# Kernel tuning notes

Hardware: AMD Instinct MI355X
Metric: run time of the kernel (lower is better)

Reference implementation:

```python
import jax, jax.numpy as jnp
import numpy as np

D = 512
H = 8
DV = D // H  # 64
NEG_INF = -1e30


def setup_inputs() -> dict:
    key = jax.random.key(0)
    ks = jax.random.split(key, 10)
    B, S = 4, 2048
    x = jax.random.normal(ks[0], (B, D, S), dtype=jnp.float32)
    mask = jnp.ones((B, S), dtype=jnp.float32)
    s = 1.0 / np.sqrt(D)
    sv = 1.0 / np.sqrt(D)
    # per-head Linear(d -> dv) weights stacked: [H, dv, d] (torch Linear layout W @ x)
    Wq = jax.random.uniform(ks[1], (H, DV, D), jnp.float32, -s, s)
    bq = jax.random.uniform(ks[2], (H, DV), jnp.float32, -s, s)
    Wk = jax.random.uniform(ks[3], (H, DV, D), jnp.float32, -s, s)
    bk = jax.random.uniform(ks[4], (H, DV), jnp.float32, -s, s)
    Wv = jax.random.uniform(ks[5], (H, DV, D), jnp.float32, -s, s)
    bv = jax.random.uniform(ks[6], (H, DV), jnp.float32, -s, s)
    W0 = jax.random.uniform(ks[7], (D, D), jnp.float32, -sv, sv)
    b0 = jax.random.uniform(ks[8], (D,), jnp.float32, -sv, sv)
    return {"x": x, "mask": mask, "Wq": Wq, "bq": bq, "Wk": Wk, "bk": bk,
            "Wv": Wv, "bv": bv, "W0": W0, "b0": b0}


def reference(x, mask, Wq, bq, Wk, bk, Wv, bv, W0, b0):
    # x: [B, d, S] -> xt: [B, S, d]
    xt = jnp.transpose(x, (0, 2, 1))
    # fused per-head projections: [B, H, S, dv]
    q = jnp.einsum('bsd,hed->bhse', xt, Wq) + bq[None, :, None, :]
    k = jnp.einsum('bsd,hed->bhse', xt, Wk) + bk[None, :, None, :]
    v = jnp.einsum('bsd,hed->bhse', xt, Wv) + bv[None, :, None, :]
    dv = q.shape[-1]
    scores = jnp.einsum('bhse,bhte->bhst', q, k) * (1.0 / np.sqrt(dv))
    # mask_logits (QANet style): keep where mask==1, else -1e30; mask over key dim
    h_mask = mask[:, None, None, :]  # [B,1,1,S]
    scores = scores * h_mask + (1.0 - h_mask) * NEG_INF
    p = jax.nn.softmax(scores, axis=-1)
    # zero out fully-masked query rows via v_mask on query dim
    p = p * mask[:, None, :, None]
    out = jnp.einsum('bhst,bhte->bhse', p, v)  # [B,H,S,dv]
    # concat heads along feature dim -> [B, S, d]
    B, _, S, _ = out.shape
    heads = jnp.transpose(out, (0, 2, 1, 3)).reshape(B, S, -1)
    y = heads @ W0.T + b0  # output projection
    return jnp.transpose(y, (0, 2, 1))  # [B, d, S]
```

## Files before the change

kernel.cpp:

```cpp
#include <hip/hip_runtime.h>

#define B_  4
#define D_  512
#define H_  8
#define DV_ 64
#define S_  2048
#define LOG2E 1.442695041f

typedef __bf16 bf16;
typedef bf16  bf16x8 __attribute__((ext_vector_type(8)));
typedef bf16  bf16x4 __attribute__((ext_vector_type(4)));
typedef float f32x4  __attribute__((ext_vector_type(4)));

#define MFMA(a, b, c) __builtin_amdgcn_mfma_f32_16x16x32_bf16((a), (b), (c), 0, 0, 0)

#define GLOAD_LDS(g, l)                                                     \
    __builtin_amdgcn_global_load_lds(                                       \
        (const __attribute__((address_space(1))) void*)(g),                 \
        (__attribute__((address_space(3))) void*)(l), 16, 0, 0)

#define WAIT_VMCNT(n)                                                       \
    __builtin_amdgcn_s_waitcnt(((n) & 15) | (((n) >> 4) << 14) | (7 << 4) | (15 << 8))

__global__ __launch_bounds__(256) void prep(
    const float* __restrict__ x, const float* __restrict__ Wq,
    const float* __restrict__ Wk, const float* __restrict__ Wv,
    const float* __restrict__ W0, bf16* __restrict__ xb, bf16* __restrict__ Wb) {
    const int bid = blockIdx.x;
    if (bid < 4096) {
        __shared__ float tile[32][33];
        const int sblk = bid % 64;
        const int dblk = (bid / 64) % 16;
        const int b    = bid / 1024;
        const int d0 = dblk * 32, s0 = sblk * 32;
        const int tx = threadIdx.x & 31;
        const int ty = threadIdx.x >> 5;
        const float* xp = x + (size_t)b * D_ * S_;
#pragma unroll
        for (int i = 0; i < 32; i += 8)
            tile[ty + i][tx] = xp[(size_t)(d0 + ty + i) * S_ + s0 + tx];
        __syncthreads();
        bf16* xbp = xb + ((size_t)b * S_ + s0) * D_ + d0;
        const int srow = threadIdx.x >> 3;
        const int d4   = (threadIdx.x & 7) * 4;
        bf16x4 hv;
#pragma unroll
        for (int j = 0; j < 4; ++j) hv[j] = (bf16)tile[d4 + j][srow];
        *(bf16x4*)&xbp[(size_t)srow * D_ + d4] = hv;
    } else {
        const int f0 = ((bid - 4096) * 256 + threadIdx.x) * 16;
        const int src = f0 >> 18;
        const int off = f0 & 262143;
        const float* W = (src == 0) ? Wq : (src == 1) ? Wk : (src == 2) ? Wv : W0;
        float4 v0 = *(const float4*)&W[off];
        float4 v1 = *(const float4*)&W[off + 4];
        float4 v2 = *(const float4*)&W[off + 8];
        float4 v3 = *(const float4*)&W[off + 12];
        bf16x8 h0 = {(bf16)v0.x, (bf16)v0.y, (bf16)v0.z, (bf16)v0.w,
                     (bf16)v1.x, (bf16)v1.y, (bf16)v1.z, (bf16)v1.w};
        bf16x8 h1 = {(bf16)v2.x, (bf16)v2.y, (bf16)v2.z, (bf16)v2.w,
                     (bf16)v3.x, (bf16)v3.y, (bf16)v3.z, (bf16)v3.w};
        *(bf16x8*)&Wb[f0]     = h0;
        *(bf16x8*)&Wb[f0 + 8] = h1;
    }
}

__global__ __launch_bounds__(256) void gemm_qkv(
    const bf16* __restrict__ A, const bf16* __restrict__ Wb,
    const float* __restrict__ bq, const float* __restrict__ bk,
    const float* __restrict__ bv,
    bf16* __restrict__ Q, bf16* __restrict__ K, bf16* __restrict__ Vt) {
    __shared__ union {
        struct { bf16 A[8192]; bf16 B[8192]; } s;
        bf16 T[128][132];
    } sm;

    const int tid = threadIdx.x;
    const int w = tid >> 6, lane = tid & 63;
    const int m16 = lane & 15, quad = lane >> 4;
    const int wr = w & 1, wc = w >> 1;

    const int bid  = (blockIdx.x & 7) * 96 + (blockIdx.x >> 3);
    const int nblk = bid % 12;
    const int mblk = bid / 12;
    const int m0 = mblk * 128, n0 = nblk * 128;

    f32x4 acc[4][4];
#pragma unroll
    for (int i = 0; i < 4; ++i)
#pragma unroll
        for (int j = 0; j < 4; ++j) acc[i][j] = (f32x4){0.f, 0.f, 0.f, 0.f};

    for (int k0 = 0; k0 < D_; k0 += 64) {
        __syncthreads();
#pragma unroll
        for (int i = 0; i < 4; ++i) {
            const int c  = w * 4 + i;
            const int mt = c >> 1, kk = c & 1;
            const int row = mt * 16 + m16;
            const int col = k0 + kk * 32 + quad * 8;
            GLOAD_LDS(&A[(size_t)(m0 + row) * D_ + col],  &sm.s.A[(c * 64 + lane) * 8]);
            GLOAD_LDS(&Wb[(size_t)(n0 + row) * D_ + col], &sm.s.B[(c * 64 + lane) * 8]);
        }
        __syncthreads();
#pragma unroll
        for (int kk = 0; kk < 2; ++kk) {
            bf16x8 af[4], bfv[4];
#pragma unroll
            for (int t = 0; t < 4; ++t) {
                af[t]  = *(const bf16x8*)&sm.s.A[(((wr * 4 + t) * 2 + kk) * 64 + lane) * 8];
                bfv[t] = *(const bf16x8*)&sm.s.B[(((wc * 4 + t) * 2 + kk) * 64 + lane) * 8];
            }
#pragma unroll
            for (int mt = 0; mt < 4; ++mt)
#pragma unroll
                for (int nt = 0; nt < 4; ++nt)
                    acc[mt][nt] = MFMA(af[mt], bfv[nt], acc[mt][nt]);
        }
    }

    const int proj = n0 >> 9;
    const float* bias = (proj == 0) ? bq : (proj == 1) ? bk : bv;

    if (proj == 2) {
#pragma unroll
        for (int mt = 0; mt < 4; ++mt)
#pragma unroll
            for (int nt = 0; nt < 4; ++nt) {
                const int nr = (n0 + wc * 64 + nt * 16 + m16) & 511;
                const int h = nr >> 6, e = nr & 63;
                const float bia = bias[nr];
                const int srow = m0 + wr * 64 + mt * 16 + quad * 4;
                const int b = srow >> 11, s = srow & 2047;
                const int s2 = (s & ~31) | (quad * 8 + (mt & 1) * 4);
                bf16x4 hv;
#pragma unroll
                for (int r = 0; r < 4; ++r) hv[r] = (bf16)(acc[mt][nt][r] + bia);
                *(bf16x4*)&Vt[(((size_t)b * H_ + h) * DV_ + e) * S_ + s2] = hv;
            }
    } else {
        __syncthreads();
#pragma unroll
        for (int mt = 0; mt < 4; ++mt)
#pragma unroll
            for (int nt = 0; nt < 4; ++nt) {
                const int nloc = wc * 64 + nt * 16 + m16;
                const float bia = bias[(n0 + nloc) & 511];
#pragma unroll
                for (int r = 0; r < 4; ++r)
                    sm.T[wr * 64 + mt * 16 + quad * 4 + r][nloc] =
                        (bf16)(acc[mt][nt][r] + bia);
            }
        __syncthreads();
        const int rloc = tid >> 1, cb = (tid & 1) * 64;
        const int M = m0 + rloc, b = M >> 11, s = M & 2047;
        const int nrb = (n0 + cb) & 511;
        const int h = nrb >> 6;
        bf16* dst = ((proj == 0) ? Q : K) + (((size_t)b * H_ + h) * S_ + s) * DV_;
#pragma unroll
        for (int u = 0; u < 8; ++u)
            *(bf16x8*)&dst[u * 8] = *(const bf16x8*)&sm.T[rloc][cb + u * 8];
    }
}

__global__ __launch_bounds__(256, 2) void flash_attn(
    const bf16* __restrict__ Q, const bf16* __restrict__ K, const bf16* __restrict__ Vt,
    const float* __restrict__ mask, bf16* __restrict__ heads) {
    __shared__ union {
        struct {
            bf16 Kl[2][4][2048];
            bf16 Vl[2][4][2048];
            float Ms[2048];
        } s;
        struct { float O[64][65]; float L[64]; } red;
    } sm;

    const int bid  = blockIdx.x;
    const int bidx = (bid & 7) * 128 + (bid >> 3);
    const int qblk = bidx & 31;
    const int h    = (bidx >> 5) & 7;
    const int b    = bidx >> 8;
    const int q0   = qblk * 64;

    const int tid = threadIdx.x;
    const int w = tid >> 6, lane = tid & 63;
    const int m16 = lane & 15, quad = lane >> 4;

    const bf16* Qp = Q  + ((size_t)b * H_ + h) * S_ * DV_;
    const bf16* Kp = K  + ((size_t)b * H_ + h) * S_ * DV_;
    const bf16* Vp = Vt + ((size_t)b * H_ + h) * DV_ * S_;
    const float* mp = mask + (size_t)b * S_;

    const int krow = lane >> 3;
    const int kcol = ((lane & 7) ^ krow) * 8;
    const int vrow = lane >> 2;
    const int vcol = ((lane & 3) ^ (vrow & 3)) * 8;

#pragma unroll
    for (int p = 0; p < 2; ++p) {
        const float4 mv = *(const float4*)&mp[(p * 256 + tid) * 4];
        f32x4 t = {mv.x * LOG2E, mv.y * LOG2E, mv.z * LOG2E, mv.w * LOG2E};
        *(f32x4*)&sm.s.Ms[(p * 256 + tid) * 4] = t;
    }

    bf16x8 qf[4][2];
#pragma unroll
    for (int qt = 0; qt < 4; ++qt)
#pragma unroll
        for (int kk = 0; kk < 2; ++kk) {
            bf16x8 v = *(const bf16x8*)&Qp[(size_t)(q0 + qt * 16 + m16) * DV_ +
                                           kk * 32 + quad * 8];
#pragma unroll
            for (int i = 0; i < 8; ++i) v[i] = (bf16)((float)v[i] * 0.125f);
            qf[qt][kk] = v;
        }

    bf16x8 ones;
#pragma unroll
    for (int i = 0; i < 8; ++i) ones[i] = (bf16)1.0f;

    f32x4 o[4][4];
    f32x4 lacc[4];
#pragma unroll
    for (int mt = 0; mt < 4; ++mt)
#pragma unroll
        for (int qt = 0; qt < 4; ++qt) o[mt][qt] = (f32x4){0.f, 0.f, 0.f, 0.f};
#pragma unroll
    for (int qt = 0; qt < 4; ++qt) lacc[qt] = (f32x4){0.f, 0.f, 0.f, 0.f};

    {
        const int tw = w * 32;
#pragma unroll
        for (int p = 0; p < 4; ++p)
            GLOAD_LDS(&Kp[(size_t)(tw + p * 8 + krow) * DV_ + kcol],
                      &sm.s.Kl[0][w][(p * 64 + lane) * 8]);
#pragma unroll
        for (int p = 0; p < 4; ++p)
            GLOAD_LDS(&Vp[(size_t)(p * 16 + vrow) * S_ + tw + vcol],
                      &sm.s.Vl[0][w][(p * 64 + lane) * 8]);
    }
    __syncthreads();

    for (int i = 0; i < 16; ++i) {
        const int tw = i * 128 + w * 32;
        if (i < 15) {
            const int twn = tw + 128;
            const int nb = (i + 1) & 1;
#pragma unroll
            for (int p = 0; p < 4; ++p)
                GLOAD_LDS(&Kp[(size_t)(twn + p * 8 + krow) * DV_ + kcol],
                          &sm.s.Kl[nb][w][(p * 64 + lane) * 8]);
#pragma unroll
            for (int p = 0; p < 4; ++p)
                GLOAD_LDS(&Vp[(size_t)(p * 16 + vrow) * S_ + twn + vcol],
                          &sm.s.Vl[nb][w][(p * 64 + lane) * 8]);
            WAIT_VMCNT(12);
        } else {
            WAIT_VMCNT(4);
        }
        __builtin_amdgcn_sched_barrier(0);
        const int buf = i & 1;

        bf16x8 kf[2][2];
#pragma unroll
        for (int tt = 0; tt < 2; ++tt)
#pragma unroll
            for (int kk = 0; kk < 2; ++kk)
                kf[tt][kk] = *(const bf16x8*)&sm.s.Kl[buf][w][
                    ((tt * 16 + m16) * 8 + ((kk * 4 + quad) ^ (m16 & 7))) * 8];
        const f32x4 m2a = *(const f32x4*)&sm.s.Ms[tw + quad * 4];
        const f32x4 m2b = *(const f32x4*)&sm.s.Ms[tw + 16 + quad * 4];

        f32x4 sc[2][4];
#pragma unroll
        for (int tt = 0; tt < 2; ++tt)
#pragma unroll
            for (int qt = 0; qt < 4; ++qt) sc[tt][qt] = (f32x4){0.f, 0.f, 0.f, 0.f};
        __builtin_amdgcn_s_setprio(1);
#pragma unroll
        for (int kk = 0; kk < 2; ++kk)
#pragma unroll
            for (int tt = 0; tt < 2; ++tt)
#pragma unroll
                for (int qt = 0; qt < 4; ++qt)
                    sc[tt][qt] = MFMA(kf[tt][kk], qf[qt][kk], sc[tt][qt]);
        __builtin_amdgcn_s_setprio(0);

        f32x4 ngA, ngB;
#pragma unroll
        for (int r = 0; r < 4; ++r) {
            ngA[r] = (m2a[r] - LOG2E) * 8e29f;
            ngB[r] = (m2b[r] - LOG2E) * 8e29f;
        }
        bf16x8 pf[4];
#pragma unroll
        for (int qt = 0; qt < 4; ++qt)
#pragma unroll
            for (int r = 0; r < 4; ++r) {
                pf[qt][r]     = (bf16)__builtin_amdgcn_exp2f(
                    __builtin_fmaf(sc[0][qt][r], m2a[r], ngA[r]));
                pf[qt][4 + r] = (bf16)__builtin_amdgcn_exp2f(
                    __builtin_fmaf(sc[1][qt][r], m2b[r], ngB[r]));
            }

#pragma unroll
        for (int qt = 0; qt < 4; ++qt) lacc[qt] = MFMA(ones, pf[qt], lacc[qt]);

        if (i < 15) WAIT_VMCNT(8);
        else        WAIT_VMCNT(0);
        __builtin_amdgcn_sched_barrier(0);

        bf16x8 vf[4];
#pragma unroll
        for (int mt = 0; mt < 4; ++mt)
            vf[mt] = *(const bf16x8*)&sm.s.Vl[buf][w][
                ((mt * 16 + m16) * 4 + (quad ^ (m16 & 3))) * 8];

        __builtin_amdgcn_s_setprio(1);
#pragma unroll
        for (int mt = 0; mt < 4; ++mt)
#pragma unroll
            for (int qt = 0; qt < 4; ++qt) o[mt][qt] = MFMA(vf[mt], pf[qt], o[mt][qt]);
        __builtin_amdgcn_s_setprio(0);
    }

    __syncthreads();
#pragma unroll
    for (int ww = 0; ww < 4; ++ww) {
        if (w == ww) {
#pragma unroll
            for (int mt = 0; mt < 4; ++mt)
#pragma unroll
                for (int qt = 0; qt < 4; ++qt)
#pragma unroll
                    for (int r = 0; r < 4; ++r) {
                        float* slot = &sm.red.O[mt * 16 + quad * 4 + r][qt * 16 + m16];
                        *slot = (ww == 0) ? o[mt][qt][r] : (*slot + o[mt][qt][r]);
                    }
            if (quad == 0)
#pragma unroll
                for (int qt = 0; qt < 4; ++qt) {
                    float* ls = &sm.red.L[qt * 16 + m16];
                    *ls = (ww == 0) ? lacc[qt][0] : (*ls + lacc[qt][0]);
                }
        }
        __syncthreads();
    }

    const int ql = tid >> 2, ec = (tid & 3) * 16;
    const float l  = sm.red.L[ql];
    const float qm = mp[q0 + ql];
    const float inv = qm / l;
    bf16x8 hv[2];
#pragma unroll
    for (int c = 0; c < 2; ++c)
#pragma unroll
        for (int i = 0; i < 8; ++i)
            hv[c][i] = (bf16)(sm.red.O[ec + c * 8 + i][ql] * inv);
    bf16* dst = &heads[((size_t)b * S_ + q0 + ql) * D_ + h * DV_ + ec];
    *(bf16x8*)(dst)     = hv[0];
    *(bf16x8*)(dst + 8) = hv[1];
}

__global__ __launch_bounds__(512) void gemm_out(
    const bf16* __restrict__ A, const bf16* __restrict__ Wb,
    const float* __restrict__ b0, float* __restrict__ outp) {
    __shared__ bf16 Asl[8192];
    __shared__ bf16 Bsl[8192];

    const int tid = threadIdx.x;
    const int w = tid >> 6, lane = tid & 63;
    const int m16 = lane & 15, quad = lane >> 4;
    const int wr = w & 1, wc = w >> 1;

    const int bid  = (blockIdx.x & 7) * 32 + (blockIdx.x >> 3);
    const int nblk = bid & 3;
    const int mblk = bid >> 2;
    const int m0 = mblk * 128, n0 = nblk * 128;

    f32x4 acc[4][2];
#pragma unroll
    for (int i = 0; i < 4; ++i)
#pragma unroll
        for (int j = 0; j < 2; ++j) acc[i][j] = (f32x4){0.f, 0.f, 0.f, 0.f};

    for (int k0 = 0; k0 < D_; k0 += 64) {
        __syncthreads();
        {
            const int cb = (w & 3) * 4;
#pragma unroll
            for (int i = 0; i < 4; ++i) {
                const int c  = cb + i;
                const int mt = c >> 1, kk = c & 1;
                const int row = mt * 16 + m16;
                const int col = k0 + kk * 32 + quad * 8;
                if (w < 4)
                    GLOAD_LDS(&A[(size_t)(m0 + row) * D_ + col],
                              &Asl[(c * 64 + lane) * 8]);
                else
                    GLOAD_LDS(&Wb[(size_t)(1536 + n0 + row) * D_ + col],
                              &Bsl[(c * 64 + lane) * 8]);
            }
        }
        __syncthreads();
#pragma unroll
        for (int kk = 0; kk < 2; ++kk) {
            bf16x8 af[4], bfv[2];
#pragma unroll
            for (int t = 0; t < 4; ++t)
                af[t]  = *(const bf16x8*)&Asl[(((wr * 4 + t) * 2 + kk) * 64 + lane) * 8];
#pragma unroll
            for (int nt = 0; nt < 2; ++nt)
                bfv[nt] = *(const bf16x8*)&Bsl[(((wc * 2 + nt) * 2 + kk) * 64 + lane) * 8];
#pragma unroll
            for (int mt = 0; mt < 4; ++mt)
#pragma unroll
                for (int nt = 0; nt < 2; ++nt)
                    acc[mt][nt] = MFMA(af[mt], bfv[nt], acc[mt][nt]);
        }
    }

#pragma unroll
    for (int mt = 0; mt < 4; ++mt)
#pragma unroll
        for (int nt = 0; nt < 2; ++nt) {
            const int n = n0 + wc * 32 + nt * 16 + m16;
            const float bia = b0[n];
            const int srow = m0 + wr * 64 + mt * 16 + quad * 4;
            const int b = srow >> 11, s = srow & 2047;
            float4 vv;
            vv.x = acc[mt][nt][0] + bia;
            vv.y = acc[mt][nt][1] + bia;
            vv.z = acc[mt][nt][2] + bia;
            vv.w = acc[mt][nt][3] + bia;
            *(float4*)&outp[((size_t)b * D_ + n) * S_ + s] = vv;
        }
}

extern "C" void kernel_launch(void* const* d_in, const int* in_sizes, int n_in,
                              void* d_out, int out_size, void* d_ws, size_t ws_size,
                              hipStream_t stream) {
    const float* x    = (const float*)d_in[0];
    const float* mask = (const float*)d_in[1];
    const float* Wq   = (const float*)d_in[2];
    const float* bq   = (const float*)d_in[3];
    const float* Wk   = (const float*)d_in[4];
    const float* bk   = (const float*)d_in[5];
    const float* Wv   = (const float*)d_in[6];
    const float* bv   = (const float*)d_in[7];
    const float* W0   = (const float*)d_in[8];
    const float* b0   = (const float*)d_in[9];
    float* out = (float*)d_out;

    char* ws = (char*)d_ws;
    const size_t SEG = (size_t)B_ * S_ * D_ * sizeof(bf16);
    bf16* xb    = (bf16*)(ws);
    bf16* Qb    = (bf16*)(ws + SEG);
    bf16* Kb    = (bf16*)(ws + 2 * SEG);
    bf16* Vt    = (bf16*)(ws + 3 * SEG);
    bf16* Wb    = (bf16*)(ws + 4 * SEG);
    bf16* heads = xb;

    prep<<<dim3(4096 + 256), dim3(256), 0, stream>>>(x, Wq, Wk, Wv, W0, xb, Wb);
    gemm_qkv<<<dim3(64 * 12), dim3(256), 0, stream>>>(xb, Wb, bq, bk, bv, Qb, Kb, Vt);
    flash_attn<<<dim3(B_ * H_ * (S_ / 64)), dim3(256), 0, stream>>>(Qb, Kb, Vt, mask, heads);
    gemm_out<<<dim3(64 * 4), dim3(512), 0, stream>>>(heads, Wb, b0, out);
}
```

Measured before the change: 194.5 us.

## Widen prep transpose tiles, use eight waves in QKV GEMM, drop setprio

The input transpose in prep now uses 64x64 tiles, float4 global loads and 8-wide bf16 stores, so it launches far fewer blocks. gemm_qkv moves to 512 threads: four waves stage the A tile and four stage the B tile, and each wave computes a 64x32 sub-tile instead of 64x64. This should raise occupancy and latency hiding in that GEMM, at the cost of more LDS traffic per MFMA. The s_setprio hints around the MFMA blocks in flash_attn are removed, which changes how waves are scheduled against each other.

```diff
diff --git a/kernel.cpp b/kernel.cpp
--- a/kernel.cpp
+++ b/kernel.cpp
@@ -27,28 +27,38 @@
     const float* __restrict__ Wk, const float* __restrict__ Wv,
     const float* __restrict__ W0, bf16* __restrict__ xb, bf16* __restrict__ Wb) {
     const int bid = blockIdx.x;
-    if (bid < 4096) {
-        __shared__ float tile[32][33];
-        const int sblk = bid % 64;
-        const int dblk = (bid / 64) % 16;
-        const int b    = bid / 1024;
-        const int d0 = dblk * 32, s0 = sblk * 32;
-        const int tx = threadIdx.x & 31;
-        const int ty = threadIdx.x >> 5;
+    if (bid < 1024) {
+        __shared__ float tile[64][65];
+        const int sblk = bid & 31;
+        const int dblk = (bid >> 5) & 7;
+        const int b    = bid >> 8;
+        const int d0 = dblk * 64, s0 = sblk * 64;
+        const int tx = threadIdx.x & 15;
+        const int ty = threadIdx.x >> 4;
         const float* xp = x + (size_t)b * D_ * S_;
 #pragma unroll
-        for (int i = 0; i < 32; i += 8)
-            tile[ty + i][tx] = xp[(size_t)(d0 + ty + i) * S_ + s0 + tx];
+        for (int i = 0; i < 64; i += 16) {
+            const float4 v = *(const float4*)&xp[(size_t)(d0 + ty + i) * S_ +
+                                                 s0 + tx * 4];
+            tile[tx * 4 + 0][ty + i] = v.x;
+            tile[tx * 4 + 1][ty + i] = v.y;
+            tile[tx * 4 + 2][ty + i] = v.z;
+            tile[tx * 4 + 3][ty + i] = v.w;
+        }
         __syncthreads();
         bf16* xbp = xb + ((size_t)b * S_ + s0) * D_ + d0;
-        const int srow = threadIdx.x >> 3;
-        const int d4   = (threadIdx.x & 7) * 4;
-        bf16x4 hv;
-#pragma unroll
-        for (int j = 0; j < 4; ++j) hv[j] = (bf16)tile[d4 + j][srow];
-        *(bf16x4*)&xbp[(size_t)srow * D_ + d4] = hv;
+        const int srow0 = threadIdx.x >> 3;
+        const int d8    = (threadIdx.x & 7) * 8;
+#pragma unroll
+        for (int i = 0; i < 2; ++i) {
+            const int srow = srow0 + i * 32;
+            bf16x8 hv;
+#pragma unroll
+            for (int j = 0; j < 8; ++j) hv[j] = (bf16)tile[srow][d8 + j];
+            *(bf16x8*)&xbp[(size_t)srow * D_ + d8] = hv;
+        }
     } else {
-        const int f0 = ((bid - 4096) * 256 + threadIdx.x) * 16;
+        const int f0 = ((bid - 1024) * 256 + threadIdx.x) * 16;
         const int src = f0 >> 18;
         const int off = f0 & 262143;
         const float* W = (src == 0) ? Wq : (src == 1) ? Wk : (src == 2) ? Wv : W0;
@@ -65,7 +75,7 @@
     }
 }
 
-__global__ __launch_bounds__(256) void gemm_qkv(
+__global__ __launch_bounds__(512) void gemm_qkv(
     const bf16* __restrict__ A, const bf16* __restrict__ Wb,
     const float* __restrict__ bq, const float* __restrict__ bk,
     const float* __restrict__ bv,
@@ -85,36 +95,44 @@
     const int mblk = bid / 12;
     const int m0 = mblk * 128, n0 = nblk * 128;
 
-    f32x4 acc[4][4];
+    f32x4 acc[4][2];
 #pragma unroll
     for (int i = 0; i < 4; ++i)
 #pragma unroll
-        for (int j = 0; j < 4; ++j) acc[i][j] = (f32x4){0.f, 0.f, 0.f, 0.f};
+        for (int j = 0; j < 2; ++j) acc[i][j] = (f32x4){0.f, 0.f, 0.f, 0.f};
 
     for (int k0 = 0; k0 < D_; k0 += 64) {
         __syncthreads();
-#pragma unroll
-        for (int i = 0; i < 4; ++i) {
-            const int c  = w * 4 + i;
-            const int mt = c >> 1, kk = c & 1;
-            const int row = mt * 16 + m16;
-            const int col = k0 + kk * 32 + quad * 8;
-            GLOAD_LDS(&A[(size_t)(m0 + row) * D_ + col],  &sm.s.A[(c * 64 + lane) * 8]);
-            GLOAD_LDS(&Wb[(size_t)(n0 + row) * D_ + col], &sm.s.B[(c * 64 + lane) * 8]);
+        {
+            const int cb = (w & 3) * 4;
+#pragma unroll
+            for (int i = 0; i < 4; ++i) {
+                const int c  = cb + i;
+                const int mt = c >> 1, kk = c & 1;
+                const int row = mt * 16 + m16;
+                const int col = k0 + kk * 32 + quad * 8;
+                if (w < 4)
+                    GLOAD_LDS(&A[(size_t)(m0 + row) * D_ + col],
+                              &sm.s.A[(c * 64 + lane) * 8]);
+                else
+                    GLOAD_LDS(&Wb[(size_t)(n0 + row) * D_ + col],
+                              &sm.s.B[(c * 64 + lane) * 8]);
+            }
         }
         __syncthreads();
 #pragma unroll
         for (int kk = 0; kk < 2; ++kk) {
-            bf16x8 af[4], bfv[4];
-#pragma unroll
-            for (int t = 0; t < 4; ++t) {
+            bf16x8 af[4], bfv[2];
+#pragma unroll
+            for (int t = 0; t < 4; ++t)
                 af[t]  = *(const bf16x8*)&sm.s.A[(((wr * 4 + t) * 2 + kk) * 64 + lane) * 8];
-                bfv[t] = *(const bf16x8*)&sm.s.B[(((wc * 4 + t) * 2 + kk) * 64 + lane) * 8];
-            }
+#pragma unroll
+            for (int nt = 0; nt < 2; ++nt)
+                bfv[nt] = *(const bf16x8*)&sm.s.B[(((wc * 2 + nt) * 2 + kk) * 64 + lane) * 8];
 #pragma unroll
             for (int mt = 0; mt < 4; ++mt)
 #pragma unroll
-                for (int nt = 0; nt < 4; ++nt)
+                for (int nt = 0; nt < 2; ++nt)
                     acc[mt][nt] = MFMA(af[mt], bfv[nt], acc[mt][nt]);
         }
     }
@@ -126,8 +144,8 @@
 #pragma unroll
         for (int mt = 0; mt < 4; ++mt)
 #pragma unroll
-            for (int nt = 0; nt < 4; ++nt) {
-                const int nr = (n0 + wc * 64 + nt * 16 + m16) & 511;
+            for (int nt = 0; nt < 2; ++nt) {
+                const int nr = (n0 + wc * 32 + nt * 16 + m16) & 511;
                 const int h = nr >> 6, e = nr & 63;
                 const float bia = bias[nr];
                 const int srow = m0 + wr * 64 + mt * 16 + quad * 4;
@@ -143,8 +161,8 @@
 #pragma unroll
         for (int mt = 0; mt < 4; ++mt)
 #pragma unroll
-            for (int nt = 0; nt < 4; ++nt) {
-                const int nloc = wc * 64 + nt * 16 + m16;
+            for (int nt = 0; nt < 2; ++nt) {
+                const int nloc = wc * 32 + nt * 16 + m16;
                 const float bia = bias[(n0 + nloc) & 511];
 #pragma unroll
                 for (int r = 0; r < 4; ++r)
@@ -152,13 +170,14 @@
                         (bf16)(acc[mt][nt][r] + bia);
             }
         __syncthreads();
-        const int rloc = tid >> 1, cb = (tid & 1) * 64;
+        const int rloc = tid >> 2, cb = (tid & 3) * 32;
         const int M = m0 + rloc, b = M >> 11, s = M & 2047;
         const int nrb = (n0 + cb) & 511;
-        const int h = nrb >> 6;
-        bf16* dst = ((proj == 0) ? Q : K) + (((size_t)b * H_ + h) * S_ + s) * DV_;
-#pragma unroll
-        for (int u = 0; u < 8; ++u)
+        const int h = nrb >> 6, eo = nrb & 63;
+        bf16* dst = ((proj == 0) ? Q : K) +
+                    (((size_t)b * H_ + h) * S_ + s) * DV_ + eo;
+#pragma unroll
+        for (int u = 0; u < 4; ++u)
             *(bf16x8*)&dst[u * 8] = *(const bf16x8*)&sm.T[rloc][cb + u * 8];
     }
 }
@@ -276,7 +295,6 @@
         for (int tt = 0; tt < 2; ++tt)
 #pragma unroll
             for (int qt = 0; qt < 4; ++qt) sc[tt][qt] = (f32x4){0.f, 0.f, 0.f, 0.f};
-        __builtin_amdgcn_s_setprio(1);
 #pragma unroll
         for (int kk = 0; kk < 2; ++kk)
 #pragma unroll
@@ -284,7 +302,6 @@
 #pragma unroll
                 for (int qt = 0; qt < 4; ++qt)
                     sc[tt][qt] = MFMA(kf[tt][kk], qf[qt][kk], sc[tt][qt]);
-        __builtin_amdgcn_s_setprio(0);
 
         f32x4 ngA, ngB;
 #pragma unroll
@@ -316,12 +333,10 @@
             vf[mt] = *(const bf16x8*)&sm.s.Vl[buf][w][
                 ((mt * 16 + m16) * 4 + (quad ^ (m16 & 3))) * 8];
 
-        __builtin_amdgcn_s_setprio(1);
 #pragma unroll
         for (int mt = 0; mt < 4; ++mt)
 #pragma unroll
             for (int qt = 0; qt < 4; ++qt) o[mt][qt] = MFMA(vf[mt], pf[qt], o[mt][qt]);
-        __builtin_amdgcn_s_setprio(0);
     }
 
     __syncthreads();
@@ -461,8 +476,8 @@
     bf16* Wb    = (bf16*)(ws + 4 * SEG);
     bf16* heads = xb;
 
-    prep<<<dim3(4096 + 256), dim3(256), 0, stream>>>(x, Wq, Wk, Wv, W0, xb, Wb);
-    gemm_qkv<<<dim3(64 * 12), dim3(256), 0, stream>>>(xb, Wb, bq, bk, bv, Qb, Kb, Vt);
+    prep<<<dim3(1024 + 256), dim3(256), 0, stream>>>(x, Wq, Wk, Wv, W0, xb, Wb);
+    gemm_qkv<<<dim3(64 * 12), dim3(512), 0, stream>>>(xb, Wb, bq, bk, bv, Qb, Kb, Vt);
     flash_attn<<<dim3(B_ * H_ * (S_ / 64)), dim3(256), 0, stream>>>(Qb, Kb, Vt, mask, heads);
     gemm_out<<<dim3(64 * 4), dim3(512), 0, stream>>>(heads, Wb, b0, out);
 }
```

Measured after the change: 191.8 us. About the same (-1.4%).
